# Kernel optimization log

Hardware: AMD Instinct MI355X
Metric: run time of the kernel (lower is better)

Reference implementation:

```python
import jax, jax.numpy as jnp
import numpy as np

VOCAB = 100000
EMB = 256
HID = 512
HDIR = HID // 2
T = 10            # tagset size
START = 8
STOP = 9
S = 4096          # sequence length
NEG = -10000.0


def setup_inputs() -> dict:
    key = jax.random.key(0)
    ks = jax.random.split(key, 16)
    sentence = jax.random.randint(ks[0], (S,), 0, VOCAB)
    emb = jax.random.normal(ks[1], (VOCAB, EMB), dtype=jnp.float32) * 0.02
    s = 1.0 / np.sqrt(HDIR).astype(np.float32)

    def lstm_weights(k):
        k1, k2, k3, k4 = jax.random.split(k, 4)
        return (
            jax.random.uniform(k1, (4 * HDIR, EMB), jnp.float32, -s, s),
            jax.random.uniform(k2, (4 * HDIR, HDIR), jnp.float32, -s, s),
            jax.random.uniform(k3, (4 * HDIR,), jnp.float32, -s, s),
            jax.random.uniform(k4, (4 * HDIR,), jnp.float32, -s, s),
        )

    Wih_f, Whh_f, bih_f, bhh_f = lstm_weights(ks[2])
    Wih_b, Whh_b, bih_b, bhh_b = lstm_weights(ks[3])
    so = 1.0 / np.sqrt(HID).astype(np.float32)
    W_out = jax.random.uniform(ks[4], (T, HID), jnp.float32, -so, so)
    b_out = jax.random.uniform(ks[5], (T,), jnp.float32, -so, so)
    transitions = jax.random.normal(ks[6], (T, T), dtype=jnp.float32)
    transitions = transitions.at[START, :].set(NEG).at[:, STOP].set(NEG)
    return {
        "sentence": sentence, "emb": emb,
        "Wih_f": Wih_f, "Whh_f": Whh_f, "bih_f": bih_f, "bhh_f": bhh_f,
        "Wih_b": Wih_b, "Whh_b": Whh_b, "bih_b": bih_b, "bhh_b": bhh_b,
        "W_out": W_out, "b_out": b_out, "transitions": transitions,
    }


def _lstm_dir(x, Wih, Whh, bih, bhh):
    # x: [S, EMB] -> hidden states [S, HDIR]; PyTorch gate order i,f,g,o
    b = bih + bhh
    xW = x @ Wih.T + b  # precompute input contribution: [S, 4*HDIR]

    def step(carry, xw_t):
        h, c = carry
        z = xw_t + Whh @ h
        i, f, g, o = jnp.split(z, 4)
        i = jax.nn.sigmoid(i); f = jax.nn.sigmoid(f)
        g = jnp.tanh(g); o = jax.nn.sigmoid(o)
        c = f * c + i * g
        h = o * jnp.tanh(c)
        return (h, c), h

    h0 = jnp.zeros((HDIR,), x.dtype)
    _, hs = jax.lax.scan(step, (h0, h0), xW)
    return hs


def _viterbi(feats, transitions):
    # feats: [S, T]
    def vstep(fv, feat):
        ntv = fv[None, :] + transitions        # [T(next), T(prev)]
        bp = jnp.argmax(ntv, axis=1)           # [T]
        fv_new = jnp.max(ntv, axis=1) + feat   # [T]
        return fv_new, bp

    init = jnp.full((T,), NEG, feats.dtype).at[START].set(0.0)
    fv, bps = jax.lax.scan(vstep, init, feats)
    terminal = fv + transitions[STOP]
    best = jnp.argmax(terminal)
    score = terminal[best]

    def back(tag, bp):
        return bp[tag], tag

    _, path_rev = jax.lax.scan(back, best, bps[::-1])
    return score, path_rev[::-1]


def reference(sentence, emb, Wih_f, Whh_f, bih_f, bhh_f,
              Wih_b, Whh_b, bih_b, bhh_b, W_out, b_out, transitions):
    x = emb[sentence]                                   # [S, EMB]
    h_f = _lstm_dir(x, Wih_f, Whh_f, bih_f, bhh_f)      # [S, HDIR]
    h_b = _lstm_dir(x[::-1], Wih_b, Whh_b, bih_b, bhh_b)[::-1]
    lstm_out = jnp.concatenate([h_f, h_b], axis=-1)     # [S, HID]
    feats = lstm_out @ W_out.T + b_out                  # [S, T]
    score, path = _viterbi(feats, transitions)
    return score, path
```

## Files before the change

### kernel.cpp

```cpp
#include <hip/hip_runtime.h>
#include <math.h>

#define S_LEN 4096
#define HDIRC 256
#define NTAG 10
#define START_TAG 8
#define STOP_TAG 9
#define NEGV -10000.0f

#define XW_OFF 0UL
#define XW_SZ  (2UL * S_LEN * 1024)
#define HS_OFF (XW_OFF + XW_SZ)
#define HS_SZ  (2UL * S_LEN * 256)
#define WT_OFF (HS_OFF + HS_SZ)
#define WT_SZ  (2UL * 256 * 1024)
#define FE_OFF (WT_OFF + WT_SZ)
#define FE_SZ  ((size_t)S_LEN * NTAG)
#define RING_OFF (FE_OFF + FE_SZ)
#define RING_SZ (2UL * 16 * 2 * 256 * 2)

#define BAR_LDS() asm volatile("s_waitcnt lgkmcnt(0)\n\ts_barrier" ::: "memory")

__global__ void transpose_wih(const float* __restrict__ wf,
                              const float* __restrict__ wb,
                              float* __restrict__ wT) {
    __shared__ float tile[32][33];
    const float* src = blockIdx.z ? wb : wf;
    float* dst = wT + (size_t)blockIdx.z * 256 * 1024;
    int x = blockIdx.x * 32 + threadIdx.x;
    int y = blockIdx.y * 32 + threadIdx.y;
    tile[threadIdx.y][threadIdx.x] = src[y * 256 + x];
    __syncthreads();
    int ko = blockIdx.x * 32 + threadIdx.y;
    int ro = blockIdx.y * 32 + threadIdx.x;
    dst[(size_t)ko * 1024 + ro] = tile[threadIdx.x][threadIdx.y];
}

__global__ __launch_bounds__(256) void xw_gemm(
    const int* __restrict__ sent, const float* __restrict__ emb,
    const float* __restrict__ wT,
    const float* __restrict__ bih_f, const float* __restrict__ bhh_f,
    const float* __restrict__ bih_b, const float* __restrict__ bhh_b,
    float* __restrict__ xw) {
    int dir = blockIdx.y;
    int t0 = blockIdx.x * 16;
    int tid = threadIdx.x;
    __shared__ __align__(16) float xs[16][256];
    for (int i = 0; i < 16; ++i) {
        int t = t0 + i;
        int pos = dir ? (S_LEN - 1 - t) : t;
        int idx = sent[pos];
        xs[i][tid] = emb[(size_t)idx * 256 + tid];
    }
    __syncthreads();
    const float* w = wT + (size_t)dir * 256 * 1024;
    const float* bi = dir ? bih_b : bih_f;
    const float* bh = dir ? bhh_b : bhh_f;
    float4 bv;
    bv.x = bi[4 * tid + 0] + bh[4 * tid + 0];
    bv.y = bi[4 * tid + 1] + bh[4 * tid + 1];
    bv.z = bi[4 * tid + 2] + bh[4 * tid + 2];
    bv.w = bi[4 * tid + 3] + bh[4 * tid + 3];
    float4 acc[16];
#pragma unroll
    for (int i = 0; i < 16; ++i) acc[i] = bv;
    for (int k4 = 0; k4 < 64; ++k4) {
        float4 w0 = ((const float4*)(w + (size_t)(4 * k4 + 0) * 1024))[tid];
        float4 w1 = ((const float4*)(w + (size_t)(4 * k4 + 1) * 1024))[tid];
        float4 w2 = ((const float4*)(w + (size_t)(4 * k4 + 2) * 1024))[tid];
        float4 w3 = ((const float4*)(w + (size_t)(4 * k4 + 3) * 1024))[tid];
#pragma unroll
        for (int i = 0; i < 16; ++i) {
            float4 xv = *(const float4*)&xs[i][4 * k4];
            acc[i].x = fmaf(w0.x, xv.x, acc[i].x);
            acc[i].y = fmaf(w0.y, xv.x, acc[i].y);
            acc[i].z = fmaf(w0.z, xv.x, acc[i].z);
            acc[i].w = fmaf(w0.w, xv.x, acc[i].w);
            acc[i].x = fmaf(w1.x, xv.y, acc[i].x);
            acc[i].y = fmaf(w1.y, xv.y, acc[i].y);
            acc[i].z = fmaf(w1.z, xv.y, acc[i].z);
            acc[i].w = fmaf(w1.w, xv.y, acc[i].w);
            acc[i].x = fmaf(w2.x, xv.z, acc[i].x);
            acc[i].y = fmaf(w2.y, xv.z, acc[i].y);
            acc[i].z = fmaf(w2.z, xv.z, acc[i].z);
            acc[i].w = fmaf(w2.w, xv.z, acc[i].w);
            acc[i].x = fmaf(w3.x, xv.w, acc[i].x);
            acc[i].y = fmaf(w3.y, xv.w, acc[i].y);
            acc[i].z = fmaf(w3.z, xv.w, acc[i].z);
            acc[i].w = fmaf(w3.w, xv.w, acc[i].w);
        }
    }
#pragma unroll
    for (int i = 0; i < 16; ++i)
        ((float4*)(xw + ((size_t)dir * S_LEN + t0 + i) * 1024))[tid] = acc[i];
}

__global__ __launch_bounds__(256, 1) void lstm_rec(
    const float* __restrict__ whh_f, const float* __restrict__ whh_b,
    const float* __restrict__ xw, float* __restrict__ hs,
    unsigned long long* __restrict__ ring) {
    int blk = blockIdx.x;
    int dir = blk >> 4;
    int b = blk & 15;
    int tid = threadIdx.x;
    int g = tid >> 6;
    int lane = tid & 63;
    int v = lane >> 2;
    int u = lane & 3;

    const float* whh = dir ? whh_b : whh_f;
    float4 w[4][4];
#pragma unroll
    for (int j = 0; j < 4; ++j)
#pragma unroll
        for (int i = 0; i < 4; ++i)
            w[j][i] = *(const float4*)(whh +
                (size_t)(g * 256 + b * 16 + 4 * u + j) * 256 + 16 * v + 4 * i);
#pragma unroll
    for (int j = 0; j < 4; ++j)
#pragma unroll
        for (int i = 0; i < 4; ++i)
            asm volatile("" : "+v"(w[j][i].x), "+v"(w[j][i].y),
                              "+v"(w[j][i].z), "+v"(w[j][i].w));

    const float* xwd = xw + (size_t)dir * S_LEN * 1024;
    float* hsd = hs + (size_t)dir * S_LEN * 256;
    unsigned long long* ringd = ring + (size_t)dir * 16 * 2 * 256;

    __shared__ __align__(16) float hbf[320];
    __shared__ __align__(16) float zpart[1056];
    for (int i = tid; i < 320; i += 256) hbf[i] = 0.f;
    float c = 0.f;
    int crow = (lane >> 4) * 256 + b * 16 + (lane & 15);
    float xw_cur = (g == 0) ? xwd[crow] : 0.f;
    __syncthreads();

    for (int t = 0; t < S_LEN; ++t) {
        const float4* hb4 = (const float4*)hbf + v * 5;
        float4 h0 = hb4[0], h1 = hb4[1], h2 = hb4[2], h3 = hb4[3];
        float s0, s1, s2, s3;
        {
            float4 a0, a1, a2, a3;
            a0.x = w[0][0].x * h0.x; a0.y = w[0][0].y * h0.y;
            a0.z = w[0][0].z * h0.z; a0.w = w[0][0].w * h0.w;
            a1.x = w[1][0].x * h0.x; a1.y = w[1][0].y * h0.y;
            a1.z = w[1][0].z * h0.z; a1.w = w[1][0].w * h0.w;
            a2.x = w[2][0].x * h0.x; a2.y = w[2][0].y * h0.y;
            a2.z = w[2][0].z * h0.z; a2.w = w[2][0].w * h0.w;
            a3.x = w[3][0].x * h0.x; a3.y = w[3][0].y * h0.y;
            a3.z = w[3][0].z * h0.z; a3.w = w[3][0].w * h0.w;

            a0.x = fmaf(w[0][1].x, h1.x, a0.x); a0.y = fmaf(w[0][1].y, h1.y, a0.y);
            a0.z = fmaf(w[0][1].z, h1.z, a0.z); a0.w = fmaf(w[0][1].w, h1.w, a0.w);
            a1.x = fmaf(w[1][1].x, h1.x, a1.x); a1.y = fmaf(w[1][1].y, h1.y, a1.y);
            a1.z = fmaf(w[1][1].z, h1.z, a1.z); a1.w = fmaf(w[1][1].w, h1.w, a1.w);
            a2.x = fmaf(w[2][1].x, h1.x, a2.x); a2.y = fmaf(w[2][1].y, h1.y, a2.y);
            a2.z = fmaf(w[2][1].z, h1.z, a2.z); a2.w = fmaf(w[2][1].w, h1.w, a2.w);
            a3.x = fmaf(w[3][1].x, h1.x, a3.x); a3.y = fmaf(w[3][1].y, h1.y, a3.y);
            a3.z = fmaf(w[3][1].z, h1.z, a3.z); a3.w = fmaf(w[3][1].w, h1.w, a3.w);

            a0.x = fmaf(w[0][2].x, h2.x, a0.x); a0.y = fmaf(w[0][2].y, h2.y, a0.y);
            a0.z = fmaf(w[0][2].z, h2.z, a0.z); a0.w = fmaf(w[0][2].w, h2.w, a0.w);
            a1.x = fmaf(w[1][2].x, h2.x, a1.x); a1.y = fmaf(w[1][2].y, h2.y, a1.y);
            a1.z = fmaf(w[1][2].z, h2.z, a1.z); a1.w = fmaf(w[1][2].w, h2.w, a1.w);
            a2.x = fmaf(w[2][2].x, h2.x, a2.x); a2.y = fmaf(w[2][2].y, h2.y, a2.y);
            a2.z = fmaf(w[2][2].z, h2.z, a2.z); a2.w = fmaf(w[2][2].w, h2.w, a2.w);
            a3.x = fmaf(w[3][2].x, h2.x, a3.x); a3.y = fmaf(w[3][2].y, h2.y, a3.y);
            a3.z = fmaf(w[3][2].z, h2.z, a3.z); a3.w = fmaf(w[3][2].w, h2.w, a3.w);

            a0.x = fmaf(w[0][3].x, h3.x, a0.x); a0.y = fmaf(w[0][3].y, h3.y, a0.y);
            a0.z = fmaf(w[0][3].z, h3.z, a0.z); a0.w = fmaf(w[0][3].w, h3.w, a0.w);
            a1.x = fmaf(w[1][3].x, h3.x, a1.x); a1.y = fmaf(w[1][3].y, h3.y, a1.y);
            a1.z = fmaf(w[1][3].z, h3.z, a1.z); a1.w = fmaf(w[1][3].w, h3.w, a1.w);
            a2.x = fmaf(w[2][3].x, h3.x, a2.x); a2.y = fmaf(w[2][3].y, h3.y, a2.y);
            a2.z = fmaf(w[2][3].z, h3.z, a2.z); a2.w = fmaf(w[2][3].w, h3.w, a2.w);
            a3.x = fmaf(w[3][3].x, h3.x, a3.x); a3.y = fmaf(w[3][3].y, h3.y, a3.y);
            a3.z = fmaf(w[3][3].z, h3.z, a3.z); a3.w = fmaf(w[3][3].w, h3.w, a3.w);

            s0 = (a0.x + a0.y) + (a0.z + a0.w);
            s1 = (a1.x + a1.y) + (a1.z + a1.w);
            s2 = (a2.x + a2.y) + (a2.z + a2.w);
            s3 = (a3.x + a3.y) + (a3.z + a3.w);
        }
        *(float4*)&zpart[g * 264 + v * 16 + u * 4] = make_float4(s0, s1, s2, s3);
        BAR_LDS();

        if (g == 0) {
            int g2 = lane >> 4, s = lane & 15;
            const float* zp = &zpart[g2 * 264 + s];
            float z = xw_cur;
#pragma unroll
            for (int vv = 0; vv < 16; ++vv) z += zp[vv * 16];
            int tn = (t + 1 < S_LEN) ? t + 1 : t;
            float xw_next = xwd[(size_t)tn * 1024 + crow];
            float act = (g2 == 2) ? tanhf(z) : 1.f / (1.f + expf(-z));
            float fg = __shfl(act, (lane & 15) + 16, 64);
            float gg = __shfl(act, (lane & 15) + 32, 64);
            float og = __shfl(act, (lane & 15) + 48, 64);
            unsigned int want = (unsigned int)(t + 1);
            if (lane < 16) {
                c = fmaf(fg, c, act * gg);
                float h = og * tanhf(c);
                unsigned long long pk = ((unsigned long long)want << 32) |
                                        (unsigned long long)__float_as_uint(h);
                unsigned long long* pd = ringd + (size_t)(t & 1) * 256 + b * 16 + lane;
#pragma unroll
                for (int cns = 0; cns < 16; ++cns)
                    __hip_atomic_store(pd + (size_t)cns * 512, pk,
                                       __ATOMIC_RELAXED, __HIP_MEMORY_SCOPE_AGENT);
                hsd[(size_t)t * 256 + b * 16 + lane] = h;
            }
            unsigned long long* own = ringd + (size_t)b * 512 + (size_t)(t & 1) * 256;
            unsigned long long v0, v1, v2, v3;
            for (;;) {
                v0 = __hip_atomic_load(&own[lane], __ATOMIC_RELAXED, __HIP_MEMORY_SCOPE_AGENT);
                v1 = __hip_atomic_load(&own[lane + 64], __ATOMIC_RELAXED, __HIP_MEMORY_SCOPE_AGENT);
                v2 = __hip_atomic_load(&own[lane + 128], __ATOMIC_RELAXED, __HIP_MEMORY_SCOPE_AGENT);
                v3 = __hip_atomic_load(&own[lane + 192], __ATOMIC_RELAXED, __HIP_MEMORY_SCOPE_AGENT);
                bool ok = ((unsigned int)(v0 >> 32) == want) &
                          ((unsigned int)(v1 >> 32) == want) &
                          ((unsigned int)(v2 >> 32) == want) &
                          ((unsigned int)(v3 >> 32) == want);
                if (__all(ok)) break;
            }
            int sl = lane & 15, ch = lane >> 4;
            hbf[(ch + 0) * 20 + sl]  = __uint_as_float((unsigned int)v0);
            hbf[(ch + 4) * 20 + sl]  = __uint_as_float((unsigned int)v1);
            hbf[(ch + 8) * 20 + sl]  = __uint_as_float((unsigned int)v2);
            hbf[(ch + 12) * 20 + sl] = __uint_as_float((unsigned int)v3);
            xw_cur = xw_next;
        }
        BAR_LDS();
    }
}

__global__ __launch_bounds__(64) void feats_k(const float* __restrict__ hs,
                                              const float* __restrict__ wout,
                                              const float* __restrict__ bout,
                                              float* __restrict__ feats) {
    int t = blockIdx.x, tau = blockIdx.y, lane = threadIdx.x;
    const float* hf = hs + (size_t)t * 256;
    const float* hbk = hs + (size_t)S_LEN * 256 + (size_t)(S_LEN - 1 - t) * 256;
    const float* w = wout + (size_t)tau * 512;
    float s = 0.f;
#pragma unroll
    for (int m = 0; m < 4; ++m) s = fmaf(w[lane + 64 * m], hf[lane + 64 * m], s);
#pragma unroll
    for (int m = 0; m < 4; ++m) s = fmaf(w[256 + lane + 64 * m], hbk[lane + 64 * m], s);
#pragma unroll
    for (int off = 32; off > 0; off >>= 1) s += __shfl_down(s, off, 64);
    if (lane == 0) feats[(size_t)t * NTAG + tau] = s + bout[tau];
}

__global__ __launch_bounds__(64) void viterbi_k(const float* __restrict__ feats,
                                                const float* __restrict__ trans,
                                                float* __restrict__ out) {
    __shared__ float fstage[128 * NTAG];
    __shared__ unsigned char bp[S_LEN * NTAG];
    __shared__ float path[S_LEN];
    __shared__ float fvbuf[NTAG];
    __shared__ float term[NTAG];
    int tid = threadIdx.x;
    float tr[NTAG];
    float trstop = 0.f;
    if (tid < NTAG) {
#pragma unroll
        for (int j = 0; j < NTAG; ++j) tr[j] = trans[tid * NTAG + j];
        trstop = trans[STOP_TAG * NTAG + tid];
    }
    float fv = (tid == START_TAG) ? 0.f : NEGV;
    for (int t0 = 0; t0 < S_LEN; t0 += 128) {
        __syncthreads();
        for (int i = tid; i < 128 * NTAG; i += 64) fstage[i] = feats[(size_t)t0 * NTAG + i];
        __syncthreads();
        for (int tt = 0; tt < 128; ++tt) {
            int t = t0 + tt;
            if (tid < NTAG) fvbuf[tid] = fv;
            __syncthreads();
            if (tid < NTAG) {
                float best = -3.4e38f; int bj = 0;
#pragma unroll
                for (int j = 0; j < NTAG; ++j) {
                    float v = fvbuf[j] + tr[j];
                    if (v > best) { best = v; bj = j; }
                }
                bp[t * NTAG + tid] = (unsigned char)bj;
                fv = best + fstage[tt * NTAG + tid];
            }
            __syncthreads();
        }
    }
    if (tid < NTAG) term[tid] = fv + trstop;
    __syncthreads();
    if (tid == 0) {
        float best = -3.4e38f; int bi = 0;
#pragma unroll
        for (int i = 0; i < NTAG; ++i) {
            float v = term[i];
            if (v > best) { best = v; bi = i; }
        }
        out[0] = best;
        int tag = bi;
        for (int t = S_LEN - 1; t >= 0; --t) {
            path[t] = (float)tag;
            tag = bp[t * NTAG + tag];
        }
    }
    __syncthreads();
    for (int i = tid; i < S_LEN; i += 64) out[1 + i] = path[i];
}

extern "C" void kernel_launch(void* const* d_in, const int* in_sizes, int n_in,
                              void* d_out, int out_size, void* d_ws, size_t ws_size,
                              hipStream_t stream) {
    const int* sent = (const int*)d_in[0];
    const float* emb = (const float*)d_in[1];
    const float* wih_f = (const float*)d_in[2];
    const float* whh_f = (const float*)d_in[3];
    const float* bih_f = (const float*)d_in[4];
    const float* bhh_f = (const float*)d_in[5];
    const float* wih_b = (const float*)d_in[6];
    const float* whh_b = (const float*)d_in[7];
    const float* bih_b = (const float*)d_in[8];
    const float* bhh_b = (const float*)d_in[9];
    const float* wout = (const float*)d_in[10];
    const float* bout = (const float*)d_in[11];
    const float* trans = (const float*)d_in[12];

    float* ws = (float*)d_ws;
    float* xw = ws + XW_OFF;
    float* hs = ws + HS_OFF;
    float* wT = ws + WT_OFF;
    float* fe = ws + FE_OFF;
    unsigned long long* ring = (unsigned long long*)(ws + RING_OFF);

    hipLaunchKernelGGL(transpose_wih, dim3(8, 32, 2), dim3(32, 32), 0, stream,
                       wih_f, wih_b, wT);
    hipLaunchKernelGGL(xw_gemm, dim3(S_LEN / 16, 2), dim3(256), 0, stream,
                       sent, emb, wT, bih_f, bhh_f, bih_b, bhh_b, xw);
    hipLaunchKernelGGL(lstm_rec, dim3(32), dim3(256), 0, stream,
                       whh_f, whh_b, xw, hs, ring);
    hipLaunchKernelGGL(feats_k, dim3(S_LEN, NTAG), dim3(64), 0, stream,
                       hs, wout, bout, fe);
    hipLaunchKernelGGL(viterbi_k, dim3(1), dim3(64), 0, stream,
                       fe, trans, (float*)d_out);
}
```

Measured before the change: 7.569 ms.

## Place recurrent blocks on one XCD and use shared fast-path h exchange

Launches 128 blocks and keeps only those with blockIdx%8 in {0,1}, so each direction's 16 blocks land on one XCD under round-robin dispatch. The 16-way replicated ring stores are replaced by a single shared slot per step, polled with sc0 loads that hit the shared L2. A fallback path periodically republishes to and polls a slow agent-scope ring in case blocks are not co-located. This depends on the undocumented assumption that blocks are assigned to XCDs round-robin, and adds extra idle blocks and fallback complexity.

```diff
diff --git a/kernel.cpp b/kernel.cpp
--- a/kernel.cpp
+++ b/kernel.cpp
@@ -16,8 +16,10 @@
 #define WT_SZ  (2UL * 256 * 1024)
 #define FE_OFF (WT_OFF + WT_SZ)
 #define FE_SZ  ((size_t)S_LEN * NTAG)
-#define RING_OFF (FE_OFF + FE_SZ)
-#define RING_SZ (2UL * 16 * 2 * 256 * 2)
+#define SLOW_OFF (FE_OFF + FE_SZ)
+#define SLOW_SZ (2UL * 2 * 256 * 2)
+#define FAST_OFF (SLOW_OFF + SLOW_SZ)
+#define FAST_SZ (2UL * 2 * 256 * 2)
 
 #define BAR_LDS() asm volatile("s_waitcnt lgkmcnt(0)\n\ts_barrier" ::: "memory")
 
@@ -98,10 +100,12 @@
 __global__ __launch_bounds__(256, 1) void lstm_rec(
     const float* __restrict__ whh_f, const float* __restrict__ whh_b,
     const float* __restrict__ xw, float* __restrict__ hs,
-    unsigned long long* __restrict__ ring) {
-    int blk = blockIdx.x;
-    int dir = blk >> 4;
-    int b = blk & 15;
+    unsigned long long* __restrict__ slowr, unsigned long long* __restrict__ fastr) {
+    int bid = blockIdx.x;
+    int xs8 = bid & 7;
+    if (xs8 > 1) return;
+    int dir = xs8;
+    int b = bid >> 3;
     int tid = threadIdx.x;
     int g = tid >> 6;
     int lane = tid & 63;
@@ -125,12 +129,14 @@
 
     const float* xwd = xw + (size_t)dir * S_LEN * 1024;
     float* hsd = hs + (size_t)dir * S_LEN * 256;
-    unsigned long long* ringd = ring + (size_t)dir * 16 * 2 * 256;
+    unsigned long long* slowd = slowr + (size_t)dir * 512;
+    unsigned long long* fastd = fastr + (size_t)dir * 512;
 
     __shared__ __align__(16) float hbf[320];
     __shared__ __align__(16) float zpart[1056];
     for (int i = tid; i < 320; i += 256) hbf[i] = 0.f;
     float c = 0.f;
+    unsigned long long pk = 0, pk_prev = 0;
     int crow = (lane >> 4) * 256 + b * 16 + (lane & 15);
     float xw_cur = (g == 0) ? xwd[crow] : 0.f;
     __syncthreads();
@@ -198,36 +204,66 @@
             float gg = __shfl(act, (lane & 15) + 32, 64);
             float og = __shfl(act, (lane & 15) + 48, 64);
             unsigned int want = (unsigned int)(t + 1);
+            unsigned long long* fsl = fastd + (size_t)(t & 1) * 256;
+            unsigned long long* ssl = slowd + (size_t)(t & 1) * 256;
+            unsigned long long* sslo = slowd + (size_t)((t & 1) ^ 1) * 256;
             if (lane < 16) {
                 c = fmaf(fg, c, act * gg);
                 float h = og * tanhf(c);
-                unsigned long long pk = ((unsigned long long)want << 32) |
-                                        (unsigned long long)__float_as_uint(h);
-                unsigned long long* pd = ringd + (size_t)(t & 1) * 256 + b * 16 + lane;
-#pragma unroll
-                for (int cns = 0; cns < 16; ++cns)
-                    __hip_atomic_store(pd + (size_t)cns * 512, pk,
-                                       __ATOMIC_RELAXED, __HIP_MEMORY_SCOPE_AGENT);
+                pk = ((unsigned long long)want << 32) |
+                     (unsigned long long)__float_as_uint(h);
+                *(volatile unsigned long long*)&fsl[b * 16 + lane] = pk;
                 hsd[(size_t)t * 256 + b * 16 + lane] = h;
             }
-            unsigned long long* own = ringd + (size_t)b * 512 + (size_t)(t & 1) * 256;
             unsigned long long v0, v1, v2, v3;
-            for (;;) {
-                v0 = __hip_atomic_load(&own[lane], __ATOMIC_RELAXED, __HIP_MEMORY_SCOPE_AGENT);
-                v1 = __hip_atomic_load(&own[lane + 64], __ATOMIC_RELAXED, __HIP_MEMORY_SCOPE_AGENT);
-                v2 = __hip_atomic_load(&own[lane + 128], __ATOMIC_RELAXED, __HIP_MEMORY_SCOPE_AGENT);
-                v3 = __hip_atomic_load(&own[lane + 192], __ATOMIC_RELAXED, __HIP_MEMORY_SCOPE_AGENT);
-                bool ok = ((unsigned int)(v0 >> 32) == want) &
-                          ((unsigned int)(v1 >> 32) == want) &
-                          ((unsigned int)(v2 >> 32) == want) &
-                          ((unsigned int)(v3 >> 32) == want);
-                if (__all(ok)) break;
+            const unsigned long long* p0 = &fsl[lane];
+            const unsigned long long* p1 = &fsl[lane + 64];
+            const unsigned long long* p2 = &fsl[lane + 128];
+            const unsigned long long* p3 = &fsl[lane + 192];
+            for (int iter = 0;; ++iter) {
+                unsigned long long f0, f1, f2, f3;
+                asm volatile(
+                    "global_load_dwordx2 %0, %4, off sc0\n\t"
+                    "global_load_dwordx2 %1, %5, off sc0\n\t"
+                    "global_load_dwordx2 %2, %6, off sc0\n\t"
+                    "global_load_dwordx2 %3, %7, off sc0\n\t"
+                    "s_waitcnt vmcnt(0)"
+                    : "=&v"(f0), "=&v"(f1), "=&v"(f2), "=&v"(f3)
+                    : "v"(p0), "v"(p1), "v"(p2), "v"(p3)
+                    : "memory");
+                bool o0 = (unsigned int)(f0 >> 32) == want;
+                bool o1 = (unsigned int)(f1 >> 32) == want;
+                bool o2 = (unsigned int)(f2 >> 32) == want;
+                bool o3 = (unsigned int)(f3 >> 32) == want;
+                if (__all(o0 & o1 & o2 & o3)) { v0 = f0; v1 = f1; v2 = f2; v3 = f3; break; }
+                if (iter & 1) {
+                    if (lane < 16) {
+                        __hip_atomic_store(&ssl[b * 16 + lane], pk,
+                                           __ATOMIC_RELAXED, __HIP_MEMORY_SCOPE_AGENT);
+                        __hip_atomic_store(&sslo[b * 16 + lane], pk_prev,
+                                           __ATOMIC_RELAXED, __HIP_MEMORY_SCOPE_AGENT);
+                    }
+                    unsigned long long q0 = __hip_atomic_load(&ssl[lane], __ATOMIC_RELAXED, __HIP_MEMORY_SCOPE_AGENT);
+                    unsigned long long q1 = __hip_atomic_load(&ssl[lane + 64], __ATOMIC_RELAXED, __HIP_MEMORY_SCOPE_AGENT);
+                    unsigned long long q2 = __hip_atomic_load(&ssl[lane + 128], __ATOMIC_RELAXED, __HIP_MEMORY_SCOPE_AGENT);
+                    unsigned long long q3 = __hip_atomic_load(&ssl[lane + 192], __ATOMIC_RELAXED, __HIP_MEMORY_SCOPE_AGENT);
+                    if (!o0) f0 = q0;
+                    if (!o1) f1 = q1;
+                    if (!o2) f2 = q2;
+                    if (!o3) f3 = q3;
+                    o0 = (unsigned int)(f0 >> 32) == want;
+                    o1 = (unsigned int)(f1 >> 32) == want;
+                    o2 = (unsigned int)(f2 >> 32) == want;
+                    o3 = (unsigned int)(f3 >> 32) == want;
+                    if (__all(o0 & o1 & o2 & o3)) { v0 = f0; v1 = f1; v2 = f2; v3 = f3; break; }
+                }
             }
             int sl = lane & 15, ch = lane >> 4;
             hbf[(ch + 0) * 20 + sl]  = __uint_as_float((unsigned int)v0);
             hbf[(ch + 4) * 20 + sl]  = __uint_as_float((unsigned int)v1);
             hbf[(ch + 8) * 20 + sl]  = __uint_as_float((unsigned int)v2);
             hbf[(ch + 12) * 20 + sl] = __uint_as_float((unsigned int)v3);
+            pk_prev = pk;
             xw_cur = xw_next;
         }
         BAR_LDS();
@@ -332,14 +368,15 @@
     float* hs = ws + HS_OFF;
     float* wT = ws + WT_OFF;
     float* fe = ws + FE_OFF;
-    unsigned long long* ring = (unsigned long long*)(ws + RING_OFF);
+    unsigned long long* slowr = (unsigned long long*)(ws + SLOW_OFF);
+    unsigned long long* fastr = (unsigned long long*)(ws + FAST_OFF);
 
     hipLaunchKernelGGL(transpose_wih, dim3(8, 32, 2), dim3(32, 32), 0, stream,
                        wih_f, wih_b, wT);
     hipLaunchKernelGGL(xw_gemm, dim3(S_LEN / 16, 2), dim3(256), 0, stream,
                        sent, emb, wT, bih_f, bhh_f, bih_b, bhh_b, xw);
-    hipLaunchKernelGGL(lstm_rec, dim3(32), dim3(256), 0, stream,
-                       whh_f, whh_b, xw, hs, ring);
+    hipLaunchKernelGGL(lstm_rec, dim3(128), dim3(256), 0, stream,
+                       whh_f, whh_b, xw, hs, slowr, fastr);
     hipLaunchKernelGGL(feats_k, dim3(S_LEN, NTAG), dim3(64), 0, stream,
                        hs, wout, bout, fe);
     hipLaunchKernelGGL(viterbi_k, dim3(1), dim3(64), 0, stream,
```

After: 12.55 ms. 65.8% more time.
